# Kernel optimization log

Measured on AMD Instinct MI355X. Metric: run time of the kernel, lower is better.

The kernel has to match this reference:

```python
import jax, jax.numpy as jnp
import numpy as np

NUM_HEADS = 8
LN_EPS = 1e-5


def _layer_norm(x, g, b):
    mu = jnp.mean(x, axis=-1, keepdims=True)
    var = jnp.mean(jnp.square(x - mu), axis=-1, keepdims=True)
    return (x - mu) * jax.lax.rsqrt(var + LN_EPS) * g + b


def setup_inputs() -> dict:
    key = jax.random.key(0)
    ks = jax.random.split(key, 8)
    B, N, D = 8, 2048, 256
    s = 0.02
    return {
        "x": jax.random.normal(ks[0], (B, N, D), jnp.float32),
        "pos": jax.random.normal(ks[1], (B, N, 2 * D), jnp.float32),
        "mask": jax.random.randint(ks[2], (B, N), 0, 2) > 0,  # True = padded key
        "Wqkv": jax.random.normal(ks[3], (D, 3 * D), jnp.float32) * s,
        "bqkv": jnp.zeros((3 * D,), jnp.float32),
        "Wpos": jax.random.normal(ks[4], (2 * D, 2 * D), jnp.float32) * s,
        "bpos": jnp.zeros((2 * D,), jnp.float32),
        "ln1_g": jnp.ones((D,), jnp.float32),
        "ln1_b": jnp.zeros((D,), jnp.float32),
        "W1": jax.random.normal(ks[5], (D, 4 * D), jnp.float32) * s,
        "b1": jnp.zeros((4 * D,), jnp.float32),
        "W2": jax.random.normal(ks[6], (4 * D, D), jnp.float32) * s,
        "b2": jnp.zeros((D,), jnp.float32),
        "ln2_g": jnp.ones((D,), jnp.float32),
        "ln2_b": jnp.zeros((D,), jnp.float32),
    }


def reference(x, pos, mask, Wqkv, bqkv, Wpos, bpos, ln1_g, ln1_b,
              W1, b1, W2, b2, ln2_g, ln2_b):
    B, N, D = x.shape
    H = NUM_HEADS
    Dh = D // H

    qkv = x @ Wqkv + bqkv                      # [B,N,3D]
    q, k, v = jnp.split(qkv, 3, axis=-1)       # each [B,N,D]
    qk_pos = pos @ Wpos + bpos                 # [B,N,2D]
    q_pos, k_pos = jnp.split(qk_pos, 2, axis=-1)
    q = q + q_pos
    k = k + k_pos

    # [B,N,D] -> [B,H,N,Dh]
    q = q.reshape(B, N, H, Dh).transpose(0, 2, 1, 3)
    k = k.reshape(B, N, H, Dh).transpose(0, 2, 1, 3)
    v = v.reshape(B, N, H, Dh).transpose(0, 2, 1, 3)

    scores = jnp.einsum('bhqd,bhkd->bhqk', q, k) / jnp.sqrt(jnp.float32(Dh))
    scores = jnp.where(mask[:, None, None, :], -jnp.inf, scores)
    attn = jax.nn.softmax(scores, axis=-1)
    out = jnp.einsum('bhqk,bhkd->bhqd', attn, v)
    out = out.transpose(0, 2, 1, 3).reshape(B, N, D)

    h = _layer_norm(x + out, ln1_g, ln1_b)
    ffn = jax.nn.relu(h @ W1 + b1) @ W2 + b2
    return _layer_norm(h + ffn, ln2_g, ln2_b)
```

## Files before the change

### kernel.cpp

```cpp
#include <hip/hip_runtime.h>
#include <math.h>

#define BATCH 8
#define SEQ   2048
#define DIM   256
#define NHEAD 8
#define DHEAD 32
#define MROWS (BATCH*SEQ)
#define KCAT  768

typedef short bf16x8 __attribute__((ext_vector_type(8)));
typedef float f32x4  __attribute__((ext_vector_type(4)));

#define CLSCALE 0.25503485f

static __device__ __forceinline__ float exp2_raw(float x) {
    float r;
    asm("v_exp_f32 %0, %1" : "=v"(r) : "v"(x));
    return r;
}

static __device__ __forceinline__ unsigned bf16rne(float f) {
    unsigned u = __float_as_uint(f);
    return (u + 0x7FFFu + ((u >> 16) & 1u)) >> 16;
}

__global__ __launch_bounds__(256) void convcat_kernel(
    const float* __restrict__ x, const float* __restrict__ pos,
    unsigned short* __restrict__ acat, int n1, int n2)
{
    int i = blockIdx.x * 256 + threadIdx.x;
    const float* s; size_t dst; int j;
    if (i < n1) {
        j = i; s = x;
        int row = j >> 5, c8 = (j & 31) * 8;
        dst = (size_t)row * KCAT + c8;
    } else {
        j = i - n1; if (j >= n2) return; s = pos;
        int row = j >> 6, c8 = (j & 63) * 8;
        dst = (size_t)row * KCAT + 256 + c8;
    }
    float4 a = ((const float4*)s)[2 * j];
    float4 b = ((const float4*)s)[2 * j + 1];
    union { unsigned short u[8]; uint4 v; } o;
    o.u[0] = bf16rne(a.x); o.u[1] = bf16rne(a.y);
    o.u[2] = bf16rne(a.z); o.u[3] = bf16rne(a.w);
    o.u[4] = bf16rne(b.x); o.u[5] = bf16rne(b.y);
    o.u[6] = bf16rne(b.z); o.u[7] = bf16rne(b.w);
    *(uint4*)&acat[dst] = o.v;
}

__global__ __launch_bounds__(256) void wtrans_all_kernel(
    const float* __restrict__ Wqkv, const float* __restrict__ Wpos,
    const float* __restrict__ W1, const float* __restrict__ W2,
    unsigned short* __restrict__ wqk, unsigned short* __restrict__ wv,
    unsigned short* __restrict__ w1, unsigned short* __restrict__ w2)
{
    int b = blockIdx.x;
    const float* src; unsigned short* dst;
    int srcN, srcColOff, dstK, dstKOff, nbx;
    if (b < 128)      {          src = Wqkv; dst = wqk; srcN = 768;  srcColOff = 0;   dstK = 768;  dstKOff = 0;   nbx = 16; }
    else if (b < 384) { b -= 128; src = Wpos; dst = wqk; srcN = 512;  srcColOff = 0;   dstK = 768;  dstKOff = 256; nbx = 16; }
    else if (b < 448) { b -= 384; src = Wqkv; dst = wv;  srcN = 768;  srcColOff = 512; dstK = 256;  dstKOff = 0;   nbx = 8;  }
    else if (b < 704) { b -= 448; src = W1;   dst = w1;  srcN = 1024; srcColOff = 0;   dstK = 256;  dstKOff = 0;   nbx = 32; }
    else              { b -= 704; src = W2;   dst = w2;  srcN = 256;  srcColOff = 0;   dstK = 1024; dstKOff = 0;   nbx = 8;  }
    const int tn0 = (b % nbx) * 32;
    const int tk0 = (b / nbx) * 32;

    __shared__ float tile[32][33];
    const int tx = threadIdx.x & 31;
    const int ty = threadIdx.x >> 5;
    #pragma unroll
    for (int r = ty; r < 32; r += 8)
        tile[r][tx] = src[(size_t)(tk0 + r) * srcN + srcColOff + tn0 + tx];
    __syncthreads();
    #pragma unroll
    for (int r = ty; r < 32; r += 8)
        dst[(size_t)(tn0 + r) * dstK + dstKOff + tk0 + tx] =
            (unsigned short)bf16rne(tile[tx][r]);
}

template<int MODE>
static __device__ __forceinline__ void mgemm_body(
    int bx, int by,
    const unsigned short* __restrict__ A, const unsigned short* __restrict__ Wt,
    const float* __restrict__ bias, const float* __restrict__ bias2,
    float* __restrict__ C, unsigned short* __restrict__ Cb,
    int M, int K, int Nc, int lda,
    unsigned short* __restrict__ u0, unsigned short* __restrict__ u1,
    unsigned short* __restrict__ u2)
{
    const int t    = threadIdx.x;
    const int wv   = t >> 6;
    const int lane = t & 63;
    const int g    = lane >> 4;
    const int lo   = lane & 15;
    const int wr   = wv >> 1;
    const int wc   = wv & 1;
    const int r0   = by * 128 + wr * 64;
    const int c0   = bx * 128 + wc * 64;

    f32x4 acc[4][4];
    #pragma unroll
    for (int i = 0; i < 4; ++i)
        #pragma unroll
        for (int j = 0; j < 4; ++j)
            #pragma unroll
            for (int r = 0; r < 4; ++r) acc[i][j][r] = 0.f;

    const unsigned short* aP[4];
    const unsigned short* bP[4];
    #pragma unroll
    for (int i = 0; i < 4; ++i) {
        aP[i] = A  + (size_t)(r0 + 16 * i + lo) * lda + g * 8;
        bP[i] = Wt + (size_t)(c0 + 16 * i + lo) * K + g * 8;
    }

    bf16x8 aA[4], bA[4], aB[4], bB[4];
    #pragma unroll
    for (int i = 0; i < 4; ++i) {
        aA[i] = *(const bf16x8*)(aP[i]);
        bA[i] = *(const bf16x8*)(bP[i]);
    }

    for (int k0 = 0; k0 < K; k0 += 64) {
        #pragma unroll
        for (int i = 0; i < 4; ++i) {
            aB[i] = *(const bf16x8*)(aP[i] + k0 + 32);
            bB[i] = *(const bf16x8*)(bP[i] + k0 + 32);
        }
        #pragma unroll
        for (int i = 0; i < 4; ++i)
            #pragma unroll
            for (int j = 0; j < 4; ++j)
                acc[i][j] = __builtin_amdgcn_mfma_f32_16x16x32_bf16(
                    aA[i], bA[j], acc[i][j], 0, 0, 0);
        if (k0 + 64 < K) {
            #pragma unroll
            for (int i = 0; i < 4; ++i) {
                aA[i] = *(const bf16x8*)(aP[i] + k0 + 64);
                bA[i] = *(const bf16x8*)(bP[i] + k0 + 64);
            }
        }
        #pragma unroll
        for (int i = 0; i < 4; ++i)
            #pragma unroll
            for (int j = 0; j < 4; ++j)
                acc[i][j] = __builtin_amdgcn_mfma_f32_16x16x32_bf16(
                    aB[i], bB[j], acc[i][j], 0, 0, 0);
    }

    #pragma unroll
    for (int j = 0; j < 4; ++j) {
        const int col = c0 + 16 * j + lo;
        const float bs = bias[col] + ((MODE == 4) ? bias2[col] : 0.f);
        #pragma unroll
        for (int i = 0; i < 4; ++i) {
            if (MODE == 5) {
                const int row0 = r0 + 16 * i + g * 4;
                const int bb   = row0 >> 11;
                const int nn0  = row0 & (SEQ - 1);
                const int hh   = col >> 5;
                const int dh   = col & 31;
                uint2 pk;
                pk.x = bf16rne(acc[i][j][0] + bs) | (bf16rne(acc[i][j][1] + bs) << 16);
                pk.y = bf16rne(acc[i][j][2] + bs) | (bf16rne(acc[i][j][3] + bs) << 16);
                *(uint2*)&u2[(((size_t)bb * NHEAD + hh) * DHEAD + dh) * SEQ + nn0] = pk;
            } else {
                #pragma unroll
                for (int r = 0; r < 4; ++r) {
                    const int row = r0 + 16 * i + g * 4 + r;
                    float v = acc[i][j][r] + bs;
                    if (MODE == 0) {
                        C[(size_t)row * Nc + col] = v;
                    } else if (MODE == 1) {
                        Cb[(size_t)row * Nc + col] =
                            (unsigned short)bf16rne(fmaxf(v, 0.f));
                    } else {
                        const int bb = row >> 11;
                        const int nn = row & (SEQ - 1);
                        const int which = col >> 8;
                        const int d  = col & 255;
                        const int hh = d >> 5;
                        const int dh = d & 31;
                        const size_t dst =
                            (((size_t)bb * NHEAD + hh) * SEQ + nn) * DHEAD + dh;
                        if (which == 0) {
                            u0[dst] = (unsigned short)bf16rne(v * CLSCALE);
                        } else {
                            u1[dst] = (unsigned short)bf16rne(v);
                        }
                    }
                }
            }
        }
    }
}

template<int MODE>
__global__ __launch_bounds__(256, 3) void mgemm_kernel(
    const unsigned short* __restrict__ A, const unsigned short* __restrict__ Wt,
    const float* __restrict__ bias, const float* __restrict__ bias2,
    float* __restrict__ C, unsigned short* __restrict__ Cb,
    int M, int K, int Nc, int lda,
    unsigned short* __restrict__ u0, unsigned short* __restrict__ u1,
    unsigned short* __restrict__ u2)
{
    mgemm_body<MODE>(blockIdx.x, blockIdx.y, A, Wt, bias, bias2, C, Cb,
                     M, K, Nc, lda, u0, u1, u2);
}

__global__ __launch_bounds__(256, 3) void qkv_kernel(
    const unsigned short* __restrict__ acat,
    const unsigned short* __restrict__ wqk, const unsigned short* __restrict__ wv,
    const float* __restrict__ bqkv, const float* __restrict__ bpos,
    unsigned short* __restrict__ qb, unsigned short* __restrict__ kb,
    unsigned short* __restrict__ vt)
{
    const int b = blockIdx.x;
    if (b < 512) {
        mgemm_body<4>(b & 3, b >> 2, acat, wqk, bqkv, bpos, nullptr, nullptr,
                      MROWS, KCAT, 512, KCAT, qb, kb, nullptr);
    } else {
        const int b2 = b - 512;
        mgemm_body<5>(b2 & 1, b2 >> 1, acat, wv, bqkv + 512, nullptr,
                      nullptr, nullptr, MROWS, 256, 256, KCAT,
                      nullptr, nullptr, vt);
    }
}

__global__ __launch_bounds__(256) void attn_kernel(
    const unsigned short* __restrict__ Qb, const unsigned short* __restrict__ Kb,
    const unsigned short* __restrict__ Vt, const int* __restrict__ mask,
    float* __restrict__ O)
{
    __shared__ float bias_s[SEQ];
    __shared__ float T[4][32][17];

    const int t    = threadIdx.x;
    const int wv   = t >> 6;
    const int lane = t & 63;
    const int g    = lane >> 4;
    const int lo   = lane & 15;

    const int sb   = ((blockIdx.x & 7) << 6) | (blockIdx.x >> 3);
    const int bh   = sb >> 3;
    const int qblk = sb & 7;
    const int bb   = bh >> 3;
    const int hh   = bh & 7;
    const int qt   = qblk * 256 + wv * 64;

    const int* mrow = mask + bb * SEQ;
    for (int i = t; i < SEQ; i += 256)
        bias_s[i] = mrow[i] ? -3.0e38f : 0.0f;
    __syncthreads();

    const unsigned short* Qh = Qb + (size_t)bh * SEQ * 32;
    const unsigned short* Kh = Kb + (size_t)bh * SEQ * 32;
    const unsigned short* Vh = Vt + (size_t)bh * 32 * SEQ;

    bf16x8 qf[4];
    #pragma unroll
    for (int i = 0; i < 4; ++i)
        qf[i] = *(const bf16x8*)&Qh[(size_t)(qt + 16 * i + lo) * 32 + g * 8];

    f32x4 acc[4][2];
    #pragma unroll
    for (int i = 0; i < 4; ++i)
        #pragma unroll
        for (int hf = 0; hf < 2; ++hf)
            #pragma unroll
            for (int r = 0; r < 4; ++r) acc[i][hf][r] = 0.f;
    float l[4] = {0.f, 0.f, 0.f, 0.f};

    const int a0 = ((((g & 1) << 5) + lo) << 2);
    const int a1 = a0 + 64;

    for (int k0 = 0; k0 < SEQ; k0 += 64) {
        bf16x8 kf[4], vf[4];
        #pragma unroll
        for (int c = 0; c < 4; ++c)
            kf[c] = *(const bf16x8*)&Kh[(size_t)(k0 + c * 16 + lo) * 32 + g * 8];
        vf[0] = *(const bf16x8*)&Vh[(size_t)lo * SEQ + k0 + g * 8];
        vf[1] = *(const bf16x8*)&Vh[(size_t)(16 + lo) * SEQ + k0 + g * 8];
        vf[2] = *(const bf16x8*)&Vh[(size_t)lo * SEQ + k0 + 32 + g * 8];
        vf[3] = *(const bf16x8*)&Vh[(size_t)(16 + lo) * SEQ + k0 + 32 + g * 8];

        f32x4 cb[4];
        #pragma unroll
        for (int c = 0; c < 4; ++c)
            cb[c] = *(const f32x4*)&bias_s[k0 + c * 16 + 4 * g];

        #pragma unroll
        for (int i = 0; i < 4; ++i) {
            f32x4 s[4];
            __builtin_amdgcn_s_setprio(1);
            #pragma unroll
            for (int c = 0; c < 4; ++c)
                s[c] = __builtin_amdgcn_mfma_f32_16x16x32_bf16(
                    kf[c], qf[i], cb[c], 0, 0, 0);
            __builtin_amdgcn_s_setprio(0);

            unsigned wA[4], wB[4];
            float tl = 0.f;
            #pragma unroll
            for (int c = 0; c < 4; ++c) {
                float p0 = exp2_raw(s[c][0]);
                float p1 = exp2_raw(s[c][1]);
                float p2 = exp2_raw(s[c][2]);
                float p3 = exp2_raw(s[c][3]);
                tl += (p0 + p1) + (p2 + p3);
                asm("v_cvt_pk_bf16_f32 %0, %1, %2"
                    : "=v"(wA[c]) : "v"(p0), "v"(p1));
                asm("v_cvt_pk_bf16_f32 %0, %1, %2"
                    : "=v"(wB[c]) : "v"(p2), "v"(p3));
            }
            l[i] += tl;

            #pragma unroll
            for (int kc = 0; kc < 2; ++kc) {
                const int c0 = 2 * kc, c1 = 2 * kc + 1;
                int x0 = __builtin_amdgcn_ds_bpermute(a0, (int)wA[c0]);
                int y0 = __builtin_amdgcn_ds_bpermute(a0, (int)wA[c1]);
                int x1 = __builtin_amdgcn_ds_bpermute(a0, (int)wB[c0]);
                int y1 = __builtin_amdgcn_ds_bpermute(a0, (int)wB[c1]);
                int x2 = __builtin_amdgcn_ds_bpermute(a1, (int)wA[c0]);
                int y2 = __builtin_amdgcn_ds_bpermute(a1, (int)wA[c1]);
                int x3 = __builtin_amdgcn_ds_bpermute(a1, (int)wB[c0]);
                int y3 = __builtin_amdgcn_ds_bpermute(a1, (int)wB[c1]);
                const bool hi2 = g >= 2;
                union { int u[4]; bf16x8 v; } pf;
                pf.u[0] = hi2 ? y0 : x0;
                pf.u[1] = hi2 ? y1 : x1;
                pf.u[2] = hi2 ? y2 : x2;
                pf.u[3] = hi2 ? y3 : x3;

                __builtin_amdgcn_s_setprio(1);
                acc[i][0] = __builtin_amdgcn_mfma_f32_16x16x32_bf16(
                    vf[2 * kc + 0], pf.v, acc[i][0], 0, 0, 0);
                acc[i][1] = __builtin_amdgcn_mfma_f32_16x16x32_bf16(
                    vf[2 * kc + 1], pf.v, acc[i][1], 0, 0, 0);
                __builtin_amdgcn_s_setprio(0);
            }
        }
    }

    #pragma unroll
    for (int i = 0; i < 4; ++i) {
        l[i] += __shfl_xor(l[i], 16);
        l[i] += __shfl_xor(l[i], 32);
        float inv = (l[i] > 0.f) ? 1.0f / l[i] : 0.f;
        #pragma unroll
        for (int hf = 0; hf < 2; ++hf)
            #pragma unroll
            for (int r = 0; r < 4; ++r)
                T[wv][hf * 16 + g * 4 + r][lo] = acc[i][hf][r] * inv;
        __syncthreads();
        #pragma unroll
        for (int p = 0; p < 2; ++p) {
            int row = p * 8 + (lane >> 3);
            int d4  = (lane & 7) * 4;
            float4 ov;
            ov.x = T[wv][d4 + 0][row];
            ov.y = T[wv][d4 + 1][row];
            ov.z = T[wv][d4 + 2][row];
            ov.w = T[wv][d4 + 3][row];
            *(float4*)&O[(size_t)(bb * SEQ + qt + i * 16 + row) * DIM + hh * 32 + d4] = ov;
        }
        __syncthreads();
    }
}

__global__ __launch_bounds__(256) void ln_kernel(
    const float* __restrict__ X, const float* __restrict__ R,
    const float* __restrict__ gam, const float* __restrict__ bet,
    float* __restrict__ Y, unsigned short* __restrict__ Yb)
{
    const int lane = threadIdx.x & 63;
    const int row  = blockIdx.x * 4 + (threadIdx.x >> 6);
    const size_t off = (size_t)row * DIM + lane * 4;

    float4 xv = *(const float4*)&X[off];
    float4 rv = *(const float4*)&R[off];
    float4 v;
    v.x = xv.x + rv.x; v.y = xv.y + rv.y;
    v.z = xv.z + rv.z; v.w = xv.w + rv.w;

    float s = (v.x + v.y) + (v.z + v.w);
    #pragma unroll
    for (int o = 1; o < 64; o <<= 1) s += __shfl_xor(s, o);
    const float mu = s * (1.f / 256.f);

    float4 d;
    d.x = v.x - mu; d.y = v.y - mu; d.z = v.z - mu; d.w = v.w - mu;
    float s2 = (d.x * d.x + d.y * d.y) + (d.z * d.z + d.w * d.w);
    #pragma unroll
    for (int o = 1; o < 64; o <<= 1) s2 += __shfl_xor(s2, o);
    const float rs = rsqrtf(s2 * (1.f / 256.f) + 1e-5f);

    float4 gv = *(const float4*)&gam[lane * 4];
    float4 bv = *(const float4*)&bet[lane * 4];
    float4 y;
    y.x = d.x * rs * gv.x + bv.x;
    y.y = d.y * rs * gv.y + bv.y;
    y.z = d.z * rs * gv.z + bv.z;
    y.w = d.w * rs * gv.w + bv.w;
    *(float4*)&Y[off] = y;

    if (Yb) {
        uint2 pk;
        pk.x = bf16rne(y.x) | (bf16rne(y.y) << 16);
        pk.y = bf16rne(y.z) | (bf16rne(y.w) << 16);
        *(uint2*)&Yb[off] = pk;
    }
}

extern "C" void kernel_launch(void* const* d_in, const int* in_sizes, int n_in,
                              void* d_out, int out_size, void* d_ws, size_t ws_size,
                              hipStream_t stream)
{
    const float* x    = (const float*)d_in[0];
    const float* pos  = (const float*)d_in[1];
    const int*   mask = (const int*)d_in[2];
    const float* Wqkv = (const float*)d_in[3];
    const float* bqkv = (const float*)d_in[4];
    const float* Wpos = (const float*)d_in[5];
    const float* bpos = (const float*)d_in[6];
    const float* ln1g = (const float*)d_in[7];
    const float* ln1b = (const float*)d_in[8];
    const float* W1   = (const float*)d_in[9];
    const float* b1   = (const float*)d_in[10];
    const float* W2   = (const float*)d_in[11];
    const float* b2   = (const float*)d_in[12];
    const float* ln2g = (const float*)d_in[13];
    const float* ln2b = (const float*)d_in[14];
    float* out = (float*)d_out;

    char* base = (char*)d_ws;
    const size_t MB = 1024 * 1024;
    const size_t SZ = (size_t)MROWS * DIM;
    unsigned short* acat = (unsigned short*)(base + 0);
    float*          ao   = (float*)(base + 0);
    unsigned short* mid  = (unsigned short*)(base + 0);
    unsigned short* qb   = (unsigned short*)(base + 34 * MB);
    unsigned short* kb   = (unsigned short*)(base + 42 * MB);
    unsigned short* vt   = (unsigned short*)(base + 58 * MB);
    unsigned short* hb   = (unsigned short*)(base + 66 * MB);
    float*          hbuf = (float*)(base + 74 * MB);
    unsigned short* wqk  = (unsigned short*)(base + 90 * MB);
    unsigned short* wv   = wqk + 512 * 768;
    unsigned short* w1   = wv + 256 * 256;
    unsigned short* w2   = w1 + 1024 * 256;
    float*          f2   = out;

    dim3 blk(256);

    convcat_kernel<<<dim3((3 * (int)(SZ / 8)) / 256), blk, 0, stream>>>(
        x, pos, acat, (int)(SZ / 8), (int)(2 * SZ / 8));
    wtrans_all_kernel<<<dim3(960), blk, 0, stream>>>(
        Wqkv, Wpos, W1, W2, wqk, wv, w1, w2);
    qkv_kernel<<<dim3(768), blk, 0, stream>>>(
        acat, wqk, wv, bqkv, bpos, qb, kb, vt);
    attn_kernel<<<dim3(BATCH * NHEAD * (SEQ / 256)), blk, 0, stream>>>(
        qb, kb, vt, mask, ao);
    ln_kernel<<<dim3(MROWS / 4), blk, 0, stream>>>(x, ao, ln1g, ln1b, hbuf, hb);
    mgemm_kernel<1><<<dim3(1024 / 128, MROWS / 128), blk, 0, stream>>>(
        hb, w1, b1, nullptr, nullptr, mid, MROWS, 256, 1024, 256,
        nullptr, nullptr, nullptr);
    mgemm_kernel<0><<<dim3(256 / 128, MROWS / 128), blk, 0, stream>>>(
        mid, w2, b2, nullptr, f2, nullptr, MROWS, 1024, 256, 1024,
        nullptr, nullptr, nullptr);
    ln_kernel<<<dim3(MROWS / 4), blk, 0, stream>>>(hbuf, f2, ln2g, ln2b, out, nullptr);
}
```

Before: 241.2 us.

## Split attention over two key halves and merge partials in LayerNorm

The attention kernel now splits each query block's key range into two halves, doubling the grid to 1024 blocks. Each block writes its unnormalized accumulator and row sums to separate buffers. A new LN1 kernel adds the two partials, divides by the combined sum, and then applies the residual and LayerNorm. The aim is more parallelism and better latency hiding in attention, paid for with extra fp32 partial-buffer traffic and a combine step. The merge stays exact only because the softmax uses no running max.

```diff
diff --git a/kernel.cpp b/kernel.cpp
--- a/kernel.cpp
+++ b/kernel.cpp
@@ -8,6 +8,7 @@
 #define DHEAD 32
 #define MROWS (BATCH*SEQ)
 #define KCAT  768
+#define SZE   ((size_t)MROWS * DIM)
 
 typedef short bf16x8 __attribute__((ext_vector_type(8)));
 typedef float f32x4  __attribute__((ext_vector_type(4)));
@@ -232,7 +233,7 @@
 __global__ __launch_bounds__(256) void attn_kernel(
     const unsigned short* __restrict__ Qb, const unsigned short* __restrict__ Kb,
     const unsigned short* __restrict__ Vt, const int* __restrict__ mask,
-    float* __restrict__ O)
+    float* __restrict__ accP, float* __restrict__ lP)
 {
     __shared__ float bias_s[SEQ];
     __shared__ float T[4][32][17];
@@ -243,12 +244,14 @@
     const int g    = lane >> 4;
     const int lo   = lane & 15;
 
-    const int sb   = ((blockIdx.x & 7) << 6) | (blockIdx.x >> 3);
-    const int bh   = sb >> 3;
-    const int qblk = sb & 7;
+    const int sb   = ((blockIdx.x & 7) << 7) | (blockIdx.x >> 3);
+    const int bh   = sb >> 4;
+    const int qblk = (sb >> 1) & 7;
+    const int kh   = sb & 1;
     const int bb   = bh >> 3;
     const int hh   = bh & 7;
     const int qt   = qblk * 256 + wv * 64;
+    const int khoff = kh * (SEQ / 2);
 
     const int* mrow = mask + bb * SEQ;
     for (int i = t; i < SEQ; i += 256)
@@ -276,7 +279,7 @@
     const int a0 = ((((g & 1) << 5) + lo) << 2);
     const int a1 = a0 + 64;
 
-    for (int k0 = 0; k0 < SEQ; k0 += 64) {
+    for (int k0 = khoff; k0 < khoff + SEQ / 2; k0 += 64) {
         bf16x8 kf[4], vf[4];
         #pragma unroll
         for (int c = 0; c < 4; ++c)
@@ -345,16 +348,18 @@
         }
     }
 
+    float* accH = accP + (size_t)kh * SZE;
     #pragma unroll
     for (int i = 0; i < 4; ++i) {
         l[i] += __shfl_xor(l[i], 16);
         l[i] += __shfl_xor(l[i], 32);
-        float inv = (l[i] > 0.f) ? 1.0f / l[i] : 0.f;
+        if (lane < 16)
+            lP[(size_t)kh * 64 * SEQ + (size_t)bh * SEQ + qt + 16 * i + lane] = l[i];
         #pragma unroll
         for (int hf = 0; hf < 2; ++hf)
             #pragma unroll
             for (int r = 0; r < 4; ++r)
-                T[wv][hf * 16 + g * 4 + r][lo] = acc[i][hf][r] * inv;
+                T[wv][hf * 16 + g * 4 + r][lo] = acc[i][hf][r];
         __syncthreads();
         #pragma unroll
         for (int p = 0; p < 2; ++p) {
@@ -365,14 +370,15 @@
             ov.y = T[wv][d4 + 1][row];
             ov.z = T[wv][d4 + 2][row];
             ov.w = T[wv][d4 + 3][row];
-            *(float4*)&O[(size_t)(bb * SEQ + qt + i * 16 + row) * DIM + hh * 32 + d4] = ov;
+            *(float4*)&accH[(size_t)(bb * SEQ + qt + i * 16 + row) * DIM + hh * 32 + d4] = ov;
         }
         __syncthreads();
     }
 }
 
-__global__ __launch_bounds__(256) void ln_kernel(
-    const float* __restrict__ X, const float* __restrict__ R,
+__global__ __launch_bounds__(256) void ln1c_kernel(
+    const float* __restrict__ X, const float* __restrict__ accP,
+    const float* __restrict__ lP,
     const float* __restrict__ gam, const float* __restrict__ bet,
     float* __restrict__ Y, unsigned short* __restrict__ Yb)
 {
@@ -380,11 +386,21 @@
     const int row  = blockIdx.x * 4 + (threadIdx.x >> 6);
     const size_t off = (size_t)row * DIM + lane * 4;
 
+    const int h   = lane >> 3;
+    const int bbv = row >> 11;
+    const int nn  = row & (SEQ - 1);
+    const size_t bhn = ((size_t)bbv * NHEAD + h) * SEQ + nn;
+    const float ls = lP[bhn] + lP[(size_t)64 * SEQ + bhn];
+    const float inv = (ls > 0.f) ? 1.0f / ls : 0.f;
+
     float4 xv = *(const float4*)&X[off];
-    float4 rv = *(const float4*)&R[off];
+    float4 a0 = *(const float4*)&accP[off];
+    float4 a1 = *(const float4*)&accP[SZE + off];
     float4 v;
-    v.x = xv.x + rv.x; v.y = xv.y + rv.y;
-    v.z = xv.z + rv.z; v.w = xv.w + rv.w;
+    v.x = xv.x + (a0.x + a1.x) * inv;
+    v.y = xv.y + (a0.y + a1.y) * inv;
+    v.z = xv.z + (a0.z + a1.z) * inv;
+    v.w = xv.w + (a0.w + a1.w) * inv;
 
     float s = (v.x + v.y) + (v.z + v.w);
     #pragma unroll
@@ -407,12 +423,47 @@
     y.w = d.w * rs * gv.w + bv.w;
     *(float4*)&Y[off] = y;
 
-    if (Yb) {
-        uint2 pk;
-        pk.x = bf16rne(y.x) | (bf16rne(y.y) << 16);
-        pk.y = bf16rne(y.z) | (bf16rne(y.w) << 16);
-        *(uint2*)&Yb[off] = pk;
-    }
+    uint2 pk;
+    pk.x = bf16rne(y.x) | (bf16rne(y.y) << 16);
+    pk.y = bf16rne(y.z) | (bf16rne(y.w) << 16);
+    *(uint2*)&Yb[off] = pk;
+}
+
+__global__ __launch_bounds__(256) void ln_kernel(
+    const float* __restrict__ X, const float* __restrict__ R,
+    const float* __restrict__ gam, const float* __restrict__ bet,
+    float* __restrict__ Y)
+{
+    const int lane = threadIdx.x & 63;
+    const int row  = blockIdx.x * 4 + (threadIdx.x >> 6);
+    const size_t off = (size_t)row * DIM + lane * 4;
+
+    float4 xv = *(const float4*)&X[off];
+    float4 rv = *(const float4*)&R[off];
+    float4 v;
+    v.x = xv.x + rv.x; v.y = xv.y + rv.y;
+    v.z = xv.z + rv.z; v.w = xv.w + rv.w;
+
+    float s = (v.x + v.y) + (v.z + v.w);
+    #pragma unroll
+    for (int o = 1; o < 64; o <<= 1) s += __shfl_xor(s, o);
+    const float mu = s * (1.f / 256.f);
+
+    float4 d;
+    d.x = v.x - mu; d.y = v.y - mu; d.z = v.z - mu; d.w = v.w - mu;
+    float s2 = (d.x * d.x + d.y * d.y) + (d.z * d.z + d.w * d.w);
+    #pragma unroll
+    for (int o = 1; o < 64; o <<= 1) s2 += __shfl_xor(s2, o);
+    const float rs = rsqrtf(s2 * (1.f / 256.f) + 1e-5f);
+
+    float4 gv = *(const float4*)&gam[lane * 4];
+    float4 bv = *(const float4*)&bet[lane * 4];
+    float4 y;
+    y.x = d.x * rs * gv.x + bv.x;
+    y.y = d.y * rs * gv.y + bv.y;
+    y.z = d.z * rs * gv.z + bv.z;
+    y.w = d.w * rs * gv.w + bv.w;
+    *(float4*)&Y[off] = y;
 }
 
 extern "C" void kernel_launch(void* const* d_in, const int* in_sizes, int n_in,
@@ -438,9 +489,8 @@
 
     char* base = (char*)d_ws;
     const size_t MB = 1024 * 1024;
-    const size_t SZ = (size_t)MROWS * DIM;
     unsigned short* acat = (unsigned short*)(base + 0);
-    float*          ao   = (float*)(base + 0);
+    float*          accP = (float*)(base + 0);
     unsigned short* mid  = (unsigned short*)(base + 0);
     unsigned short* qb   = (unsigned short*)(base + 34 * MB);
     unsigned short* kb   = (unsigned short*)(base + 42 * MB);
@@ -451,24 +501,26 @@
     unsigned short* wv   = wqk + 512 * 768;
     unsigned short* w1   = wv + 256 * 256;
     unsigned short* w2   = w1 + 1024 * 256;
+    float*          lP   = (float*)(base + 93 * MB);
     float*          f2   = out;
 
     dim3 blk(256);
 
-    convcat_kernel<<<dim3((3 * (int)(SZ / 8)) / 256), blk, 0, stream>>>(
-        x, pos, acat, (int)(SZ / 8), (int)(2 * SZ / 8));
+    convcat_kernel<<<dim3((3 * (int)(SZE / 8)) / 256), blk, 0, stream>>>(
+        x, pos, acat, (int)(SZE / 8), (int)(2 * SZE / 8));
     wtrans_all_kernel<<<dim3(960), blk, 0, stream>>>(
         Wqkv, Wpos, W1, W2, wqk, wv, w1, w2);
     qkv_kernel<<<dim3(768), blk, 0, stream>>>(
         acat, wqk, wv, bqkv, bpos, qb, kb, vt);
-    attn_kernel<<<dim3(BATCH * NHEAD * (SEQ / 256)), blk, 0, stream>>>(
-        qb, kb, vt, mask, ao);
-    ln_kernel<<<dim3(MROWS / 4), blk, 0, stream>>>(x, ao, ln1g, ln1b, hbuf, hb);
+    attn_kernel<<<dim3(1024), blk, 0, stream>>>(
+        qb, kb, vt, mask, accP, lP);
+    ln1c_kernel<<<dim3(MROWS / 4), blk, 0, stream>>>(
+        x, accP, lP, ln1g, ln1b, hbuf, hb);
     mgemm_kernel<1><<<dim3(1024 / 128, MROWS / 128), blk, 0, stream>>>(
         hb, w1, b1, nullptr, nullptr, mid, MROWS, 256, 1024, 256,
         nullptr, nullptr, nullptr);
     mgemm_kernel<0><<<dim3(256 / 128, MROWS / 128), blk, 0, stream>>>(
         mid, w2, b2, nullptr, f2, nullptr, MROWS, 1024, 256, 1024,
         nullptr, nullptr, nullptr);
-    ln_kernel<<<dim3(MROWS / 4), blk, 0, stream>>>(hbuf, f2, ln2g, ln2b, out, nullptr);
-}
+    ln_kernel<<<dim3(MROWS / 4), blk, 0, stream>>>(hbuf, f2, ln2g, ln2b, out);
+}
```

After: 243.1 us. Within noise of the previous version (+0.8%).

## Switch attention to 32x32x16 MFMA with permlane32 swap instead of bpermute

Applied to the files above, without the earlier changes.

Rewrites the attention inner loop to use 32x32x16 bf16 MFMAs over 32-key steps, producing a 32x32 score tile per query block. The P-matrix relayout for the PV MFMA now uses v_permlane32_swap instead of eight ds_bpermute calls per chunk, which avoids LDS-path traffic. The output epilogue writes float4s straight from the accumulator layout, dropping the shared transpose buffer and its barriers. The cost is larger accumulator register tiles, which may affect occupancy, and correctness depends on the 32x32 output layout matching the operand layout expected after the lane swap.

```diff
diff --git a/kernel.cpp b/kernel.cpp
--- a/kernel.cpp
+++ b/kernel.cpp
@@ -11,6 +11,7 @@
 
 typedef short bf16x8 __attribute__((ext_vector_type(8)));
 typedef float f32x4  __attribute__((ext_vector_type(4)));
+typedef float f32x16 __attribute__((ext_vector_type(16)));
 
 #define CLSCALE 0.25503485f
 
@@ -235,13 +236,12 @@
     float* __restrict__ O)
 {
     __shared__ float bias_s[SEQ];
-    __shared__ float T[4][32][17];
 
     const int t    = threadIdx.x;
     const int wv   = t >> 6;
     const int lane = t & 63;
-    const int g    = lane >> 4;
-    const int lo   = lane & 15;
+    const int h    = lane >> 5;
+    const int ql   = lane & 31;
 
     const int sb   = ((blockIdx.x & 7) << 6) | (blockIdx.x >> 3);
     const int bh   = sb >> 3;
@@ -259,115 +259,92 @@
     const unsigned short* Kh = Kb + (size_t)bh * SEQ * 32;
     const unsigned short* Vh = Vt + (size_t)bh * 32 * SEQ;
 
-    bf16x8 qf[4];
-    #pragma unroll
-    for (int i = 0; i < 4; ++i)
-        qf[i] = *(const bf16x8*)&Qh[(size_t)(qt + 16 * i + lo) * 32 + g * 8];
-
-    f32x4 acc[4][2];
-    #pragma unroll
-    for (int i = 0; i < 4; ++i)
-        #pragma unroll
-        for (int hf = 0; hf < 2; ++hf)
-            #pragma unroll
-            for (int r = 0; r < 4; ++r) acc[i][hf][r] = 0.f;
-    float l[4] = {0.f, 0.f, 0.f, 0.f};
-
-    const int a0 = ((((g & 1) << 5) + lo) << 2);
-    const int a1 = a0 + 64;
-
-    for (int k0 = 0; k0 < SEQ; k0 += 64) {
-        bf16x8 kf[4], vf[4];
-        #pragma unroll
-        for (int c = 0; c < 4; ++c)
-            kf[c] = *(const bf16x8*)&Kh[(size_t)(k0 + c * 16 + lo) * 32 + g * 8];
-        vf[0] = *(const bf16x8*)&Vh[(size_t)lo * SEQ + k0 + g * 8];
-        vf[1] = *(const bf16x8*)&Vh[(size_t)(16 + lo) * SEQ + k0 + g * 8];
-        vf[2] = *(const bf16x8*)&Vh[(size_t)lo * SEQ + k0 + 32 + g * 8];
-        vf[3] = *(const bf16x8*)&Vh[(size_t)(16 + lo) * SEQ + k0 + 32 + g * 8];
-
-        f32x4 cb[4];
-        #pragma unroll
-        for (int c = 0; c < 4; ++c)
-            cb[c] = *(const f32x4*)&bias_s[k0 + c * 16 + 4 * g];
-
-        #pragma unroll
-        for (int i = 0; i < 4; ++i) {
-            f32x4 s[4];
+    bf16x8 qf[2][2];
+    #pragma unroll
+    for (int i = 0; i < 2; ++i)
+        #pragma unroll
+        for (int dh = 0; dh < 2; ++dh)
+            qf[i][dh] = *(const bf16x8*)&Qh[(size_t)(qt + 32 * i + ql) * 32 + 16 * dh + 8 * h];
+
+    f32x16 acc[2];
+    #pragma unroll
+    for (int i = 0; i < 2; ++i)
+        #pragma unroll
+        for (int r = 0; r < 16; ++r) acc[i][r] = 0.f;
+    float l[2] = {0.f, 0.f};
+
+    for (int k0 = 0; k0 < SEQ; k0 += 32) {
+        bf16x8 kf0 = *(const bf16x8*)&Kh[(size_t)(k0 + ql) * 32 + 8 * h];
+        bf16x8 kf1 = *(const bf16x8*)&Kh[(size_t)(k0 + ql) * 32 + 16 + 8 * h];
+        bf16x8 vf0 = *(const bf16x8*)&Vh[(size_t)ql * SEQ + k0 + 8 * h];
+        bf16x8 vf1 = *(const bf16x8*)&Vh[(size_t)ql * SEQ + k0 + 16 + 8 * h];
+
+        f32x16 cbv;
+        #pragma unroll
+        for (int c = 0; c < 4; ++c) {
+            f32x4 cb = *(const f32x4*)&bias_s[k0 + 4 * h + 8 * c];
+            #pragma unroll
+            for (int e = 0; e < 4; ++e) cbv[4 * c + e] = cb[e];
+        }
+
+        #pragma unroll
+        for (int i = 0; i < 2; ++i) {
             __builtin_amdgcn_s_setprio(1);
-            #pragma unroll
-            for (int c = 0; c < 4; ++c)
-                s[c] = __builtin_amdgcn_mfma_f32_16x16x32_bf16(
-                    kf[c], qf[i], cb[c], 0, 0, 0);
+            f32x16 s = __builtin_amdgcn_mfma_f32_32x32x16_bf16(
+                kf0, qf[i][0], cbv, 0, 0, 0);
+            s = __builtin_amdgcn_mfma_f32_32x32x16_bf16(
+                kf1, qf[i][1], s, 0, 0, 0);
             __builtin_amdgcn_s_setprio(0);
 
-            unsigned wA[4], wB[4];
+            float p[16];
             float tl = 0.f;
             #pragma unroll
-            for (int c = 0; c < 4; ++c) {
-                float p0 = exp2_raw(s[c][0]);
-                float p1 = exp2_raw(s[c][1]);
-                float p2 = exp2_raw(s[c][2]);
-                float p3 = exp2_raw(s[c][3]);
-                tl += (p0 + p1) + (p2 + p3);
-                asm("v_cvt_pk_bf16_f32 %0, %1, %2"
-                    : "=v"(wA[c]) : "v"(p0), "v"(p1));
-                asm("v_cvt_pk_bf16_f32 %0, %1, %2"
-                    : "=v"(wB[c]) : "v"(p2), "v"(p3));
+            for (int r = 0; r < 16; ++r) {
+                p[r] = exp2_raw(s[r]);
+                tl += p[r];
             }
             l[i] += tl;
 
-            #pragma unroll
-            for (int kc = 0; kc < 2; ++kc) {
-                const int c0 = 2 * kc, c1 = 2 * kc + 1;
-                int x0 = __builtin_amdgcn_ds_bpermute(a0, (int)wA[c0]);
-                int y0 = __builtin_amdgcn_ds_bpermute(a0, (int)wA[c1]);
-                int x1 = __builtin_amdgcn_ds_bpermute(a0, (int)wB[c0]);
-                int y1 = __builtin_amdgcn_ds_bpermute(a0, (int)wB[c1]);
-                int x2 = __builtin_amdgcn_ds_bpermute(a1, (int)wA[c0]);
-                int y2 = __builtin_amdgcn_ds_bpermute(a1, (int)wA[c1]);
-                int x3 = __builtin_amdgcn_ds_bpermute(a1, (int)wB[c0]);
-                int y3 = __builtin_amdgcn_ds_bpermute(a1, (int)wB[c1]);
-                const bool hi2 = g >= 2;
-                union { int u[4]; bf16x8 v; } pf;
-                pf.u[0] = hi2 ? y0 : x0;
-                pf.u[1] = hi2 ? y1 : x1;
-                pf.u[2] = hi2 ? y2 : x2;
-                pf.u[3] = hi2 ? y3 : x3;
-
-                __builtin_amdgcn_s_setprio(1);
-                acc[i][0] = __builtin_amdgcn_mfma_f32_16x16x32_bf16(
-                    vf[2 * kc + 0], pf.v, acc[i][0], 0, 0, 0);
-                acc[i][1] = __builtin_amdgcn_mfma_f32_16x16x32_bf16(
-                    vf[2 * kc + 1], pf.v, acc[i][1], 0, 0, 0);
-                __builtin_amdgcn_s_setprio(0);
-            }
-        }
-    }
-
-    #pragma unroll
-    for (int i = 0; i < 4; ++i) {
-        l[i] += __shfl_xor(l[i], 16);
+            unsigned w00, w01, w10, w11, w20, w21, w30, w31;
+            asm("v_cvt_pk_bf16_f32 %0, %1, %2" : "=v"(w00) : "v"(p[0]),  "v"(p[1]));
+            asm("v_cvt_pk_bf16_f32 %0, %1, %2" : "=v"(w01) : "v"(p[2]),  "v"(p[3]));
+            asm("v_cvt_pk_bf16_f32 %0, %1, %2" : "=v"(w10) : "v"(p[4]),  "v"(p[5]));
+            asm("v_cvt_pk_bf16_f32 %0, %1, %2" : "=v"(w11) : "v"(p[6]),  "v"(p[7]));
+            asm("v_cvt_pk_bf16_f32 %0, %1, %2" : "=v"(w20) : "v"(p[8]),  "v"(p[9]));
+            asm("v_cvt_pk_bf16_f32 %0, %1, %2" : "=v"(w21) : "v"(p[10]), "v"(p[11]));
+            asm("v_cvt_pk_bf16_f32 %0, %1, %2" : "=v"(w30) : "v"(p[12]), "v"(p[13]));
+            asm("v_cvt_pk_bf16_f32 %0, %1, %2" : "=v"(w31) : "v"(p[14]), "v"(p[15]));
+            asm volatile("v_permlane32_swap_b32 %0, %1" : "+v"(w00), "+v"(w10));
+            asm volatile("v_permlane32_swap_b32 %0, %1" : "+v"(w01), "+v"(w11));
+            asm volatile("v_permlane32_swap_b32 %0, %1" : "+v"(w20), "+v"(w30));
+            asm volatile("v_permlane32_swap_b32 %0, %1" : "+v"(w21), "+v"(w31));
+            union { unsigned u[4]; bf16x8 v; } pa, pb;
+            pa.u[0] = w00; pa.u[1] = w01; pa.u[2] = w10; pa.u[3] = w11;
+            pb.u[0] = w20; pb.u[1] = w21; pb.u[2] = w30; pb.u[3] = w31;
+
+            __builtin_amdgcn_s_setprio(1);
+            acc[i] = __builtin_amdgcn_mfma_f32_32x32x16_bf16(
+                vf0, pa.v, acc[i], 0, 0, 0);
+            acc[i] = __builtin_amdgcn_mfma_f32_32x32x16_bf16(
+                vf1, pb.v, acc[i], 0, 0, 0);
+            __builtin_amdgcn_s_setprio(0);
+        }
+    }
+
+    #pragma unroll
+    for (int i = 0; i < 2; ++i) {
         l[i] += __shfl_xor(l[i], 32);
-        float inv = (l[i] > 0.f) ? 1.0f / l[i] : 0.f;
-        #pragma unroll
-        for (int hf = 0; hf < 2; ++hf)
-            #pragma unroll
-            for (int r = 0; r < 4; ++r)
-                T[wv][hf * 16 + g * 4 + r][lo] = acc[i][hf][r] * inv;
-        __syncthreads();
-        #pragma unroll
-        for (int p = 0; p < 2; ++p) {
-            int row = p * 8 + (lane >> 3);
-            int d4  = (lane & 7) * 4;
+        const float inv = (l[i] > 0.f) ? 1.0f / l[i] : 0.f;
+        const size_t rowoff = (size_t)(bb * SEQ + qt + 32 * i + ql) * DIM + hh * 32;
+        #pragma unroll
+        for (int c = 0; c < 4; ++c) {
             float4 ov;
-            ov.x = T[wv][d4 + 0][row];
-            ov.y = T[wv][d4 + 1][row];
-            ov.z = T[wv][d4 + 2][row];
-            ov.w = T[wv][d4 + 3][row];
-            *(float4*)&O[(size_t)(bb * SEQ + qt + i * 16 + row) * DIM + hh * 32 + d4] = ov;
-        }
-        __syncthreads();
+            ov.x = acc[i][4 * c + 0] * inv;
+            ov.y = acc[i][4 * c + 1] * inv;
+            ov.z = acc[i][4 * c + 2] * inv;
+            ov.w = acc[i][4 * c + 3] * inv;
+            *(float4*)&O[rowoff + 4 * h + 8 * c] = ov;
+        }
     }
 }
 
```

Measured after the change: 238.1 us (median of 2 runs). No clear change (-1.3%).
